# Kernel tuning notes

Measured on AMD Instinct MI355X. Metric: run time of the kernel, lower is better.

The kernel has to match this reference:

```python
import jax, jax.numpy as jnp
import numpy as np

RES = 7          # pooler_resolution
SR = 2           # sampling_ratio
SCALES = (1.0 / 8.0, 1.0 / 16.0, 1.0 / 32.0)
IMG = 1024.0


def roi_align_one(feat, boxes, scale):
    """torchvision roi_align (aligned=True) for one image.
    feat: [C,H,W]; boxes: [N,4] (x1,y1,x2,y2) -> [N,C,RES,RES]."""
    C, H, W = feat.shape
    N = boxes.shape[0]
    b = boxes * scale - 0.5  # aligned=True offset
    x1, y1, x2, y2 = b[:, 0], b[:, 1], b[:, 2], b[:, 3]
    bh = (y2 - y1) / RES
    bw = (x2 - x1) / RES
    # sample points within each bin: y = y1 + bh*(iy + (jy+0.5)/SR)
    grid = (jnp.arange(RES, dtype=feat.dtype)[:, None]
            + (jnp.arange(SR, dtype=feat.dtype)[None, :] + 0.5) / SR).reshape(-1)  # [RES*SR]
    ys = y1[:, None] + bh[:, None] * grid[None, :]  # [N, RES*SR]
    xs = x1[:, None] + bw[:, None] * grid[None, :]

    def prep(c, size):
        m = ((c >= -1.0) & (c <= size)).astype(feat.dtype)
        cc = jnp.clip(c, 0.0, size - 1)
        lo = jnp.minimum(jnp.floor(cc).astype(jnp.int32), size - 1)
        hi = jnp.minimum(lo + 1, size - 1)
        frac = cc - lo.astype(feat.dtype)
        return lo, hi, frac, m

    y0, y1i, ly, my = prep(ys, H)
    x0, x1i, lx, mx = prep(xs, W)
    hy, hx = 1.0 - ly, 1.0 - lx
    # gather 4 corners: result [C, N, Sy, Sx]
    f00 = feat[:, y0[:, :, None], x0[:, None, :]]
    f01 = feat[:, y0[:, :, None], x1i[:, None, :]]
    f10 = feat[:, y1i[:, :, None], x0[:, None, :]]
    f11 = feat[:, y1i[:, :, None], x1i[:, None, :]]
    val = (hy[:, :, None] * (hx[:, None, :] * f00 + lx[:, None, :] * f01)
           + ly[:, :, None] * (hx[:, None, :] * f10 + lx[:, None, :] * f11))
    val = val * (my[:, :, None] * mx[:, None, :])
    pooled = val.reshape(C, N, RES, SR, RES, SR).mean(axis=(3, 5))  # avg over samples per bin
    return pooled.transpose(1, 0, 2, 3)  # [N, C, RES, RES]


def setup_inputs() -> dict:
    key = jax.random.key(0)
    ks = jax.random.split(key, 12)
    B, N, C = 4, 512, 256
    feat_p3 = jax.random.normal(ks[0], (B, C, 128, 128), jnp.float32)
    feat_p4 = jax.random.normal(ks[1], (B, C, 64, 64), jnp.float32)
    feat_p5 = jax.random.normal(ks[2], (B, C, 32, 32), jnp.float32)
    # valid boxes inside a 1024x1024 image
    cx = jax.random.uniform(ks[3], (B, N), minval=0.0, maxval=IMG)
    cy = jax.random.uniform(ks[4], (B, N), minval=0.0, maxval=IMG)
    bw = jax.random.uniform(ks[5], (B, N), minval=16.0, maxval=256.0)
    bh = jax.random.uniform(ks[6], (B, N), minval=16.0, maxval=256.0)
    x1 = jnp.clip(cx - bw / 2, 0.0, IMG - 1.0)
    y1 = jnp.clip(cy - bh / 2, 0.0, IMG - 1.0)
    x2 = jnp.clip(cx + bw / 2, x1 + 1.0, IMG)
    y2 = jnp.clip(cy + bh / 2, y1 + 1.0, IMG)
    bbox2d = jnp.stack([x1, y1, x2, y2], axis=-1)  # [B,N,4]
    anchor_id = jax.random.randint(ks[7], (B, N, 1), 0, 9, dtype=jnp.int32)
    FLAT = C * RES * RES  # 12544
    FC = 1024
    OUT = 93
    W1 = jax.random.normal(ks[8], (FC, FLAT), jnp.float32) * 0.01
    b1 = jnp.zeros((FC,), jnp.float32)
    W2 = jax.random.normal(ks[9], (FC, FC), jnp.float32) * 0.02
    b2 = jnp.zeros((FC,), jnp.float32)
    Wp = jax.random.normal(ks[10], (OUT, FC), jnp.float32) * 0.02
    bp = jnp.zeros((OUT,), jnp.float32)
    return {"feat_p3": feat_p3, "feat_p4": feat_p4, "feat_p5": feat_p5,
            "bbox2d": bbox2d, "anchor_id": anchor_id,
            "W1": W1, "b1": b1, "W2": W2, "b2": b2, "Wp": Wp, "bp": bp}


def reference(feat_p3, feat_p4, feat_p5, bbox2d, anchor_id, W1, b1, W2, b2, Wp, bp):
    B, N = bbox2d.shape[:2]
    level = anchor_id[..., 0] // 3  # [B,N] in {0,1,2}
    feats = (feat_p3, feat_p4, feat_p5)
    # pool every proposal at every level, then pick its assigned level
    pooled = None
    for l, (scale, feat) in enumerate(zip(SCALES, feats)):
        p = jax.vmap(lambda f, bx, s=scale: roi_align_one(f, bx, s))(feat, bbox2d)  # [B,N,C,R,R]
        sel = (level == l).astype(p.dtype)[..., None, None, None]
        pooled = p * sel if pooled is None else pooled + p * sel
    x = pooled.reshape(B * N, -1)  # flatten [B*N, C*R*R]
    x = jax.nn.relu(x @ W1.T + b1)
    x = jax.nn.relu(x @ W2.T + b2)
    out = x @ Wp.T + bp
    return out.reshape(B, N, -1)  # [4, 512, 93]
```

## Files before the change

### kernel.cpp

```cpp
#include <hip/hip_runtime.h>
#include <hip/hip_bf16.h>

typedef unsigned short u16;
typedef __attribute__((ext_vector_type(8))) short short8;
typedef __attribute__((ext_vector_type(4))) float f32x4;
typedef __attribute__((ext_vector_type(4))) unsigned short us4;
typedef __attribute__((ext_vector_type(8))) _Float16 h8;

__device__ __forceinline__ u16 f32_bf16(float f) {
  union { float f; unsigned int u; } v; v.f = f;
  unsigned int r = v.u + 0x7fffu + ((v.u >> 16) & 1u);
  return (u16)(r >> 16);
}
__device__ __forceinline__ float bf16_f32(u16 h) {
  union { unsigned int u; float f; } v; v.u = ((unsigned int)h) << 16; return v.f;
}
__device__ __forceinline__ u16 f32_f16(float f) {
  union { _Float16 h; u16 u; } v; v.h = (_Float16)f; return v.u;
}
__device__ __forceinline__ h8 splat8(float f) {
  _Float16 h = (_Float16)f;
  h8 r = {h, h, h, h, h, h, h, h};
  return r;
}

__device__ __forceinline__ void load_lds16(const void* g, void* l) {
  __builtin_amdgcn_global_load_lds((const __attribute__((address_space(1))) unsigned int*)g,
                                   (__attribute__((address_space(3))) unsigned int*)l,
                                   16, 0, 0);
}

__global__ __launch_bounds__(256) void cvt_all(
    const float* __restrict__ W1, const float* __restrict__ W2,
    const float* __restrict__ Wp,
    u16* __restrict__ W1b, u16* __restrict__ W2b, u16* __restrict__ Wpb) {
  const int bid = blockIdx.x;
  const float* src; u16* dst; int i;
  if (bid < 12544)      { i = bid * 256 + threadIdx.x; src = W1; dst = W1b; }
  else if (bid < 13568) { i = (bid - 12544) * 256 + threadIdx.x; src = W2; dst = W2b; }
  else {
    i = (bid - 13568) * 256 + threadIdx.x;
    float4 v = (i * 4 < 95232) ? ((const float4*)Wp)[i] : float4{0.f, 0.f, 0.f, 0.f};
    unsigned long long pk = (unsigned long long)f32_bf16(v.x)
                          | ((unsigned long long)f32_bf16(v.y) << 16)
                          | ((unsigned long long)f32_bf16(v.z) << 32)
                          | ((unsigned long long)f32_bf16(v.w) << 48);
    ((unsigned long long*)Wpb)[i] = pk;
    return;
  }
  const float4 v = ((const float4*)src)[i];
  unsigned long long pk = (unsigned long long)f32_bf16(v.x)
                        | ((unsigned long long)f32_bf16(v.y) << 16)
                        | ((unsigned long long)f32_bf16(v.z) << 32)
                        | ((unsigned long long)f32_bf16(v.w) << 48);
  ((unsigned long long*)dst)[i] = pk;
}

__global__ __launch_bounds__(256) void transpose_feats(
    const float* __restrict__ p3, const float* __restrict__ p4, const float* __restrict__ p5,
    u16* __restrict__ t3, u16* __restrict__ t4, u16* __restrict__ t5) {
  const int bid = blockIdx.x;
  const float* src; u16* dst; int S, tile;
  if (bid < 16384)      { src = p3; dst = t3; S = 128; tile = bid; }
  else if (bid < 20480) { src = p4; dst = t4; S = 64;  tile = bid - 16384; }
  else                  { src = p5; dst = t5; S = 32;  tile = bid - 20480; }
  const int cchunk = tile & 3;
  const int fp0 = (tile >> 2) * 16;
  const int SS = S * S;
  const int b = fp0 / SS;
  const int pimg = fp0 - b * SS;
  __shared__ __align__(16) u16 lds[16 * 72];
  const int t = threadIdx.x;
  {
    const int cl = t >> 2, xv = t & 3;
    const int c = cchunk * 64 + cl;
    const float4 v = *(const float4*)(src + (size_t)(b * 256 + c) * SS + pimg + xv * 4);
    lds[(xv * 4 + 0) * 72 + cl] = f32_f16(v.x);
    lds[(xv * 4 + 1) * 72 + cl] = f32_f16(v.y);
    lds[(xv * 4 + 2) * 72 + cl] = f32_f16(v.z);
    lds[(xv * 4 + 3) * 72 + cl] = f32_f16(v.w);
  }
  __syncthreads();
  {
    const int xl = t >> 4, cg = (t & 15) * 4;
    const us4 h = *(const us4*)&lds[xl * 72 + cg];
    *(us4*)(dst + (size_t)(fp0 + xl) * 256 + cchunk * 64 + cg) = h;
  }
}

__global__ __launch_bounds__(256) void roi_pool3(
    const u16* __restrict__ t3, const u16* __restrict__ t4, const u16* __restrict__ t5,
    const float* __restrict__ bbox, const int* __restrict__ anchor,
    u16* __restrict__ X) {
  const int m = blockIdx.x;
  const int b = m >> 9;
  const int lvl = anchor[m] / 3;
  const u16* ft; int S; float scale;
  if (lvl == 0)      { ft = t3; S = 128; scale = 0.125f;   }
  else if (lvl == 1) { ft = t4; S = 64;  scale = 0.0625f;  }
  else               { ft = t5; S = 32;  scale = 0.03125f; }
  ft += (size_t)b * S * S * 256;
  const float* bx = bbox + (size_t)m * 4;
  const float x1 = bx[0] * scale - 0.5f;
  const float y1 = bx[1] * scale - 0.5f;
  const float bw = (bx[2] * scale - 0.5f - x1) * (1.0f / 7.0f);
  const float bh = (bx[3] * scale - 0.5f - y1) * (1.0f / 7.0f);
  const float fS = (float)S;

  __shared__ __align__(16) u16 xs[12544];
  const int wave = threadIdx.x >> 6, lane = threadIdx.x & 63;
  const int l = lane & 31, h = lane >> 5;
  const int cbase = l * 8;

#pragma unroll 1
  for (int it = 0; it < 7; ++it) {
    const int p = it * 8 + wave * 2 + h;
    if (p < 49) {
      const int py = p / 7, px = p - py * 7;
      h8 acc = splat8(0.0f);
#pragma unroll
      for (int sy = 0; sy < 2; ++sy) {
        const float y = y1 + bh * ((float)py + (sy ? 0.75f : 0.25f));
        const float my = (y >= -1.0f && y <= fS) ? 1.0f : 0.0f;
        const float cy = fminf(fmaxf(y, 0.0f), fS - 1.0f);
        const int y0 = (int)cy;
        const float ly = cy - (float)y0;
        const float hy = 1.0f - ly;
        const int y1i = (y0 + 1 < S) ? y0 + 1 : S - 1;
#pragma unroll
        for (int sx = 0; sx < 2; ++sx) {
          const float x = x1 + bw * ((float)px + (sx ? 0.75f : 0.25f));
          const float mx = (x >= -1.0f && x <= fS) ? 1.0f : 0.0f;
          const float cx = fminf(fmaxf(x, 0.0f), fS - 1.0f);
          const int x0 = (int)cx;
          const float lx = cx - (float)x0;
          const float hx = 1.0f - lx;
          const int x1i = (x0 + 1 < S) ? x0 + 1 : S - 1;
          const h8 f00 = *(const h8*)(ft + (size_t)(y0  * S + x0 ) * 256 + cbase);
          const h8 f01 = *(const h8*)(ft + (size_t)(y0  * S + x1i) * 256 + cbase);
          const h8 f10 = *(const h8*)(ft + (size_t)(y1i * S + x0 ) * 256 + cbase);
          const h8 f11 = *(const h8*)(ft + (size_t)(y1i * S + x1i) * 256 + cbase);
          const float msk = my * mx;
          acc += f00 * splat8(hy * hx * msk);
          acc += f01 * splat8(hy * lx * msk);
          acc += f10 * splat8(ly * hx * msk);
          acc += f11 * splat8(ly * lx * msk);
        }
      }
#pragma unroll
      for (int i = 0; i < 8; ++i)
        xs[(cbase + i) * 49 + p] = f32_bf16((float)acc[i] * 0.25f);
    }
  }
  __syncthreads();
  uint4* dst = (uint4*)(X + (size_t)m * 12544);
  const uint4* srcl = (const uint4*)xs;
  for (int i = threadIdx.x; i < 1568; i += 256) dst[i] = srcl[i];
}

__global__ __launch_bounds__(512, 2)
void gemm8_bt(const u16* __restrict__ A, int lda,
              const u16* __restrict__ B, int ldb,
              u16* __restrict__ Cpart, int M, int N,
              int mb, int nb) {
  __shared__ __align__(16) char lds[131072];
  const int tid = threadIdx.x;
  const int wave = tid >> 6, lane = tid & 63;
  const int wr = wave >> 2, wc = wave & 3;

  const int G = gridDim.x;
  const int bid = blockIdx.x;
  const int swz = (bid & 7) * (G >> 3) + (bid >> 3);
  const int x = swz % mb;
  const int rest = swz / mb;
  const int y = rest % nb;
  const int z = rest / nb;
  const int m0 = x * 256, n0 = y * 256;
  const int nt = 24 + (z < 4 ? 1 : 0);
  const int kb0 = (z * 24 + (z < 4 ? z : 4)) * 64;

  const int sb = ((lane & 7) ^ (lane >> 3)) << 4;
  const int rowb2 = 2 * (wave * 8 + (lane >> 3)) + (sb >> 6);
  const int keloff = (sb & 63) >> 1;

  const int frow = lane & 15;
  const int rh = frow >> 1;
  const int swb = ((((frow & 1) << 6) | ((lane >> 4) << 4))) ^ (rh << 4);
  const int a_rd = wr * 8192 + rh * 128 + swb;
  const int b_rd = wc * 4096 + rh * 128 + swb;

  f32x4 acc[8][4];
#pragma unroll
  for (int i = 0; i < 8; ++i)
#pragma unroll
    for (int j = 0; j < 4; ++j)
      acc[i][j] = f32x4{0.f, 0.f, 0.f, 0.f};

  auto stageAB = [&](int tile, int ph) {
    const int dst = ((tile & 1) * 2 + ph) * 16384;
    const int kel = kb0 + tile * 64 + ph * 32 + keloff;
#pragma unroll
    for (int i = 0; i < 2; ++i) {
      const u16* srcA = A + (size_t)(m0 + i * 128 + rowb2) * lda + kel;
      load_lds16(srcA, lds + dst + i * 8192 + wave * 1024);
    }
#pragma unroll
    for (int i = 0; i < 2; ++i) {
      const u16* srcB = B + (size_t)(n0 + i * 128 + rowb2) * ldb + kel;
      load_lds16(srcB, lds + 65536 + dst + i * 8192 + wave * 1024);
    }
  };

#define GPHASE(T, PH, VW, DOSTAGE)                                              \
  {                                                                             \
    asm volatile("s_waitcnt vmcnt(" VW ")" ::: "memory");                       \
    __builtin_amdgcn_s_barrier();                                               \
    __builtin_amdgcn_sched_barrier(0);                                          \
    if (DOSTAGE) stageAB((T) + 1, (PH));                                        \
    const int hb_ = (((T) & 1) * 2 + (PH)) * 16384;                             \
    short8 af[8], bf[4];                                                        \
    _Pragma("unroll")                                                           \
    for (int fi = 0; fi < 8; ++fi)                                              \
      af[fi] = *(const short8*)(lds + hb_ + a_rd + fi * 1024);                  \
    _Pragma("unroll")                                                           \
    for (int fj = 0; fj < 4; ++fj)                                              \
      bf[fj] = *(const short8*)(lds + 65536 + hb_ + b_rd + fj * 1024);          \
    __builtin_amdgcn_s_setprio(1);                                              \
    _Pragma("unroll")                                                           \
    for (int fi = 0; fi < 8; ++fi) {                                            \
      _Pragma("unroll")                                                         \
      for (int fj = 0; fj < 4; ++fj)                                            \
        acc[fi][fj] = __builtin_amdgcn_mfma_f32_16x16x32_bf16(af[fi], bf[fj],   \
                                                              acc[fi][fj], 0, 0, 0); \
    }                                                                           \
    __builtin_amdgcn_s_setprio(0);                                              \
  }

  stageAB(0, 0);
  stageAB(0, 1);
#pragma unroll 1
  for (int t = 0; t < nt - 1; ++t) {
    GPHASE(t, 0, "4", true);
    GPHASE(t, 1, "4", true);
  }
  GPHASE(nt - 1, 0, "4", false);
  GPHASE(nt - 1, 1, "0", false);
#undef GPHASE

  u16* Cp = Cpart + (size_t)z * ((size_t)M * N);
  const int rq = (lane >> 4) * 4;
  const int cq = lane & 15;
#pragma unroll
  for (int fi = 0; fi < 8; ++fi)
#pragma unroll
    for (int fj = 0; fj < 4; ++fj) {
      const int row = m0 + wr * 128 + fi * 16 + rq;
      const int col = n0 + wc * 64 + fj * 16 + cq;
#pragma unroll
      for (int q = 0; q < 4; ++q)
        Cp[(size_t)(row + q) * N + col] = f32_bf16(acc[fi][fj][q]);
    }
}

__global__ __launch_bounds__(256) void reduce_bias8(
    const u16* __restrict__ P8, const float* __restrict__ bias,
    u16* __restrict__ out) {
  const int i4 = (blockIdx.x * 256 + threadIdx.x) * 4;
  if (i4 >= 2097152) return;
  const int nb = i4 & 1023;
  float s0 = bias[nb], s1 = bias[nb + 1], s2 = bias[nb + 2], s3 = bias[nb + 3];
#pragma unroll
  for (int j = 0; j < 8; ++j) {
    const us4 v = *(const us4*)(P8 + (size_t)j * 2097152 + i4);
    s0 += bf16_f32(v.x); s1 += bf16_f32(v.y); s2 += bf16_f32(v.z); s3 += bf16_f32(v.w);
  }
  us4 o;
  o.x = f32_bf16(fmaxf(s0, 0.f)); o.y = f32_bf16(fmaxf(s1, 0.f));
  o.z = f32_bf16(fmaxf(s2, 0.f)); o.w = f32_bf16(fmaxf(s3, 0.f));
  *(us4*)(out + i4) = o;
}

template<int BM, int BN, int WGM, int WGN>
__global__ __launch_bounds__(256)
void gemm_bt_splitk(const u16* __restrict__ A, int lda,
                    const u16* __restrict__ B, int ldb,
                    float* __restrict__ Cpart, int M, int N, int Ksplit) {
  constexpr int BK = 64;
  constexpr int WM = BM / WGM, WN = BN / WGN;
  constexpr int FM = WM / 16, FN = WN / 16;
  constexpr int AITER = BM * BK / 2048;
  constexpr int BITER = BN * BK / 2048;
  __shared__ u16 Asm_[BM * BK];
  __shared__ u16 Bsm_[BN * BK];
  const int tid = threadIdx.x;
  const int wave = tid >> 6, lane = tid & 63;
  const int wr = wave / WGN, wc = wave % WGN;
  const int m0 = blockIdx.x * BM, n0 = blockIdx.y * BN;
  const int kbase0 = blockIdx.z * Ksplit;

  f32x4 acc[FM][FN];
#pragma unroll
  for (int i = 0; i < FM; ++i)
#pragma unroll
    for (int j = 0; j < FN; ++j)
      acc[i][j] = f32x4{0.0f, 0.0f, 0.0f, 0.0f};

  const int ar = tid >> 3;
  const int acsub = (tid & 7) * 8;
  const int fr = lane & 15;
  const int kq = (lane >> 4) * 8;

  for (int kt = 0; kt < Ksplit; kt += BK) {
    const int kb = kbase0 + kt;
#pragma unroll
    for (int it = 0; it < AITER; ++it) {
      const u16* src = A + (size_t)(m0 + it * 32 + ar) * lda + kb + acsub;
      load_lds16(src, (char*)Asm_ + it * 4096 + wave * 1024);
    }
#pragma unroll
    for (int it = 0; it < BITER; ++it) {
      const u16* src = B + (size_t)(n0 + it * 32 + ar) * ldb + kb + acsub;
      load_lds16(src, (char*)Bsm_ + it * 4096 + wave * 1024);
    }
    __syncthreads();
#pragma unroll
    for (int kk = 0; kk < BK; kk += 32) {
      short8 af[FM], bfr[FN];
#pragma unroll
      for (int i = 0; i < FM; ++i)
        af[i] = *(const short8*)(Asm_ + (wr * WM + i * 16 + fr) * BK + kk + kq);
#pragma unroll
      for (int j = 0; j < FN; ++j)
        bfr[j] = *(const short8*)(Bsm_ + (wc * WN + j * 16 + fr) * BK + kk + kq);
#pragma unroll
      for (int i = 0; i < FM; ++i)
#pragma unroll
        for (int j = 0; j < FN; ++j)
          acc[i][j] = __builtin_amdgcn_mfma_f32_16x16x32_bf16(af[i], bfr[j], acc[i][j], 0, 0, 0);
    }
    __syncthreads();
  }

  float* Cp = Cpart + (size_t)blockIdx.z * ((size_t)M * N);
  const int rq = (lane >> 4) * 4;
  const int cq = lane & 15;
#pragma unroll
  for (int i = 0; i < FM; ++i)
#pragma unroll
    for (int j = 0; j < FN; ++j) {
      const int row = m0 + wr * WM + i * 16 + rq;
      const int col = n0 + wc * WN + j * 16 + cq;
      float* o = Cp + (size_t)row * N + col;
#pragma unroll
      for (int q = 0; q < 4; ++q)
        o[(size_t)q * N] = acc[i][j][q];
    }
}

template<int S, bool RELU>
__global__ __launch_bounds__(256) void reduce_bias_bf16(
    const float* __restrict__ P, const float* __restrict__ bias,
    u16* __restrict__ out, int MN, int Nmask) {
  const int i = blockIdx.x * 256 + threadIdx.x;
  if (i >= MN) return;
  float s = bias[i & Nmask];
#pragma unroll
  for (int j = 0; j < S; ++j) s += P[(size_t)j * MN + i];
  if (RELU) s = fmaxf(s, 0.0f);
  out[i] = f32_bf16(s);
}

__global__ __launch_bounds__(256) void reduce_out(
    const float* __restrict__ P, const float* __restrict__ bp,
    float* __restrict__ out) {
  const int i = blockIdx.x * 256 + threadIdx.x;
  if (i >= 2048 * 93) return;
  const int mrow = i / 93;
  const int n = i - mrow * 93;
  float s = bp[n];
#pragma unroll
  for (int j = 0; j < 8; ++j) s += P[(size_t)j * (2048 * 96) + mrow * 96 + n];
  out[i] = s;
}

extern "C" void kernel_launch(void* const* d_in, const int* in_sizes, int n_in,
                              void* d_out, int out_size, void* d_ws, size_t ws_size,
                              hipStream_t stream) {
  const float* p3   = (const float*)d_in[0];
  const float* p4   = (const float*)d_in[1];
  const float* p5   = (const float*)d_in[2];
  const float* bbox = (const float*)d_in[3];
  const int*   anc  = (const int*)d_in[4];
  const float* W1   = (const float*)d_in[5];
  const float* b1   = (const float*)d_in[6];
  const float* W2   = (const float*)d_in[7];
  const float* b2   = (const float*)d_in[8];
  const float* Wp   = (const float*)d_in[9];
  const float* bp   = (const float*)d_in[10];
  float* out = (float*)d_out;

  char* ws = (char*)d_ws;
  u16* X   = (u16*)(ws);
  u16* W1b = (u16*)(ws + 51380224);
  char* R = ws + 77070336;
  u16* t3  = (u16*)(R);
  u16* t4  = (u16*)(R + 33554432);
  u16* t5  = (u16*)(R + 41943040);
  u16* W2b = (u16*)(R);
  u16* Wpb = (u16*)(R + 2097152);
  u16* H1  = (u16*)(R + 2293760);
  u16* H2  = (u16*)(R + 6488064);
  u16*   P8 = (u16*)(R + 10682368);
  float* Pf = (float*)(R + 10682368);
  (void)ws_size; (void)in_sizes; (void)n_in; (void)out_size;

  hipLaunchKernelGGL(transpose_feats, dim3(21504), dim3(256), 0, stream, p3, p4, p5, t3, t4, t5);
  hipLaunchKernelGGL(roi_pool3, dim3(2048), dim3(256), 0, stream, t3, t4, t5, bbox, anc, X);
  hipLaunchKernelGGL(cvt_all, dim3(13664), dim3(256), 0, stream, W1, W2, Wp, W1b, W2b, Wpb);
  hipLaunchKernelGGL(gemm8_bt, dim3(256), dim3(512), 0, stream,
                     X, 12544, W1b, 12544, P8, 2048, 1024, 8, 4);
  hipLaunchKernelGGL(reduce_bias8, dim3(2048), dim3(256), 0, stream, P8, b1, H1);
  hipLaunchKernelGGL((gemm_bt_splitk<128,128,2,2>), dim3(16, 8, 2), dim3(256), 0, stream,
                     H1, 1024, W2b, 1024, Pf, 2048, 1024, 512);
  hipLaunchKernelGGL((reduce_bias_bf16<2,true>), dim3(8192), dim3(256), 0, stream,
                     Pf, b2, H2, 2048 * 1024, 1023);
  hipLaunchKernelGGL((gemm_bt_splitk<128,96,4,1>), dim3(16, 1, 8), dim3(256), 0, stream,
                     H2, 1024, Wpb, 1024, Pf, 2048, 96, 128);
  hipLaunchKernelGGL(reduce_out, dim3(744), dim3(256), 0, stream, Pf, bp, out);
}
```

Baseline: 172.1 us.

## Fuse weight conversions into neighboring kernels and stage both K halves at once

The standalone weight conversion kernel is removed. The W1 bf16 conversion now runs as extra blocks of the feature-transpose kernel, and the W2/Wp conversions run as extra blocks of the first bias-reduction kernel, which cuts one launch and lets those memory-bound jobs share a grid. Separately, the main GEMM pipeline now issues both phase stages of the next K tile in the first phase and none in the second, with the wait count adjusted to match. This changes how loads overlap with MFMA work and may alter LDS hazard timing.

```diff
diff --git a/kernel.cpp b/kernel.cpp
--- a/kernel.cpp
+++ b/kernel.cpp
@@ -23,6 +23,12 @@
   h8 r = {h, h, h, h, h, h, h, h};
   return r;
 }
+__device__ __forceinline__ unsigned long long pack4bf(float4 v) {
+  return (unsigned long long)f32_bf16(v.x)
+       | ((unsigned long long)f32_bf16(v.y) << 16)
+       | ((unsigned long long)f32_bf16(v.z) << 32)
+       | ((unsigned long long)f32_bf16(v.w) << 48);
+}
 
 __device__ __forceinline__ void load_lds16(const void* g, void* l) {
   __builtin_amdgcn_global_load_lds((const __attribute__((address_space(1))) unsigned int*)g,
@@ -30,36 +36,16 @@
                                    16, 0, 0);
 }
 
-__global__ __launch_bounds__(256) void cvt_all(
-    const float* __restrict__ W1, const float* __restrict__ W2,
-    const float* __restrict__ Wp,
-    u16* __restrict__ W1b, u16* __restrict__ W2b, u16* __restrict__ Wpb) {
+__global__ __launch_bounds__(256) void transpose_w1(
+    const float* __restrict__ p3, const float* __restrict__ p4, const float* __restrict__ p5,
+    u16* __restrict__ t3, u16* __restrict__ t4, u16* __restrict__ t5,
+    const float* __restrict__ W1, u16* __restrict__ W1b) {
   const int bid = blockIdx.x;
-  const float* src; u16* dst; int i;
-  if (bid < 12544)      { i = bid * 256 + threadIdx.x; src = W1; dst = W1b; }
-  else if (bid < 13568) { i = (bid - 12544) * 256 + threadIdx.x; src = W2; dst = W2b; }
-  else {
-    i = (bid - 13568) * 256 + threadIdx.x;
-    float4 v = (i * 4 < 95232) ? ((const float4*)Wp)[i] : float4{0.f, 0.f, 0.f, 0.f};
-    unsigned long long pk = (unsigned long long)f32_bf16(v.x)
-                          | ((unsigned long long)f32_bf16(v.y) << 16)
-                          | ((unsigned long long)f32_bf16(v.z) << 32)
-                          | ((unsigned long long)f32_bf16(v.w) << 48);
-    ((unsigned long long*)Wpb)[i] = pk;
+  if (bid >= 21504) {
+    const int i = (bid - 21504) * 256 + threadIdx.x;
+    ((unsigned long long*)W1b)[i] = pack4bf(((const float4*)W1)[i]);
     return;
   }
-  const float4 v = ((const float4*)src)[i];
-  unsigned long long pk = (unsigned long long)f32_bf16(v.x)
-                        | ((unsigned long long)f32_bf16(v.y) << 16)
-                        | ((unsigned long long)f32_bf16(v.z) << 32)
-                        | ((unsigned long long)f32_bf16(v.w) << 48);
-  ((unsigned long long*)dst)[i] = pk;
-}
-
-__global__ __launch_bounds__(256) void transpose_feats(
-    const float* __restrict__ p3, const float* __restrict__ p4, const float* __restrict__ p5,
-    u16* __restrict__ t3, u16* __restrict__ t4, u16* __restrict__ t5) {
-  const int bid = blockIdx.x;
   const float* src; u16* dst; int S, tile;
   if (bid < 16384)      { src = p3; dst = t3; S = 128; tile = bid; }
   else if (bid < 20480) { src = p4; dst = t4; S = 64;  tile = bid - 16384; }
@@ -216,7 +202,7 @@
     asm volatile("s_waitcnt vmcnt(" VW ")" ::: "memory");                       \
     __builtin_amdgcn_s_barrier();                                               \
     __builtin_amdgcn_sched_barrier(0);                                          \
-    if (DOSTAGE) stageAB((T) + 1, (PH));                                        \
+    if (DOSTAGE) { stageAB((T) + 1, 0); stageAB((T) + 1, 1); }                  \
     const int hb_ = (((T) & 1) * 2 + (PH)) * 16384;                             \
     short8 af[8], bf[4];                                                        \
     _Pragma("unroll")                                                           \
@@ -241,7 +227,7 @@
 #pragma unroll 1
   for (int t = 0; t < nt - 1; ++t) {
     GPHASE(t, 0, "4", true);
-    GPHASE(t, 1, "4", true);
+    GPHASE(t, 1, "8", false);
   }
   GPHASE(nt - 1, 0, "4", false);
   GPHASE(nt - 1, 1, "0", false);
@@ -262,11 +248,24 @@
     }
 }
 
-__global__ __launch_bounds__(256) void reduce_bias8(
+__global__ __launch_bounds__(256) void reduce_cvt(
     const u16* __restrict__ P8, const float* __restrict__ bias,
-    u16* __restrict__ out) {
-  const int i4 = (blockIdx.x * 256 + threadIdx.x) * 4;
-  if (i4 >= 2097152) return;
+    u16* __restrict__ out,
+    const float* __restrict__ W2, const float* __restrict__ Wp,
+    u16* __restrict__ W2b, u16* __restrict__ Wpb) {
+  const int bid = blockIdx.x;
+  if (bid >= 3072) {
+    const int i = (bid - 3072) * 256 + threadIdx.x;
+    float4 v = (i * 4 < 95232) ? ((const float4*)Wp)[i] : float4{0.f, 0.f, 0.f, 0.f};
+    ((unsigned long long*)Wpb)[i] = pack4bf(v);
+    return;
+  }
+  if (bid >= 2048) {
+    const int i = (bid - 2048) * 256 + threadIdx.x;
+    ((unsigned long long*)W2b)[i] = pack4bf(((const float4*)W2)[i]);
+    return;
+  }
+  const int i4 = (bid * 256 + threadIdx.x) * 4;
   const int nb = i4 & 1023;
   float s0 = bias[nb], s1 = bias[nb + 1], s2 = bias[nb + 2], s3 = bias[nb + 3];
 #pragma unroll
@@ -414,12 +413,13 @@
   float* Pf = (float*)(R + 10682368);
   (void)ws_size; (void)in_sizes; (void)n_in; (void)out_size;
 
-  hipLaunchKernelGGL(transpose_feats, dim3(21504), dim3(256), 0, stream, p3, p4, p5, t3, t4, t5);
+  hipLaunchKernelGGL(transpose_w1, dim3(34048), dim3(256), 0, stream,
+                     p3, p4, p5, t3, t4, t5, W1, W1b);
   hipLaunchKernelGGL(roi_pool3, dim3(2048), dim3(256), 0, stream, t3, t4, t5, bbox, anc, X);
-  hipLaunchKernelGGL(cvt_all, dim3(13664), dim3(256), 0, stream, W1, W2, Wp, W1b, W2b, Wpb);
   hipLaunchKernelGGL(gemm8_bt, dim3(256), dim3(512), 0, stream,
                      X, 12544, W1b, 12544, P8, 2048, 1024, 8, 4);
-  hipLaunchKernelGGL(reduce_bias8, dim3(2048), dim3(256), 0, stream, P8, b1, H1);
+  hipLaunchKernelGGL(reduce_cvt, dim3(3168), dim3(256), 0, stream,
+                     P8, b1, H1, W2, Wp, W2b, Wpb);
   hipLaunchKernelGGL((gemm_bt_splitk<128,128,2,2>), dim3(16, 8, 2), dim3(256), 0, stream,
                      H1, 1024, W2b, 1024, Pf, 2048, 1024, 512);
   hipLaunchKernelGGL((reduce_bias_bf16<2,true>), dim3(8192), dim3(256), 0, stream,
```

After: 174.6 us. No clear change (+1.5%).
